# Performance work log

Measured on AMD Instinct MI355X. Metric: run time of the kernel, lower is better.

## Reference

```python
import jax, jax.numpy as jnp
import numpy as np

B, L, D, R = 8, 2048, 2048, 256
K = R if R % 2 == 1 else (R - 1 if R > 1 else 1)  # torch kernel-size rule -> 255


def setup_inputs() -> dict:
    key = jax.random.key(0)
    ks = jax.random.split(key, 6)
    x = jax.random.normal(ks[0], (B, L, D), dtype=jnp.float32)
    ln_gamma = jnp.ones((D,), jnp.float32)
    ln_beta = jnp.zeros((D,), jnp.float32)
    P_shared = jax.random.normal(ks[1], (D, R), jnp.float32) / np.float32(np.sqrt(D))
    dlt_T = jax.random.normal(ks[2], (R, R), jnp.float32) / np.float32(np.sqrt(R))
    phi_w = jax.random.normal(ks[3], (R,), jnp.float32)  # nn.Linear(1, r, bias=False) weight
    phi_bias = jnp.zeros((L, R), jnp.float32)            # created as zeros_like(phi_det)
    toep_params = jnp.ones((K,), jnp.float32) / np.float32(K)
    Wq = jax.random.normal(ks[4], (R, D), jnp.float32) / np.float32(np.sqrt(R))  # delta_Q: r->d
    bq = jnp.zeros((D,), jnp.float32)
    g_logit = jnp.array([-1.0, 0.0], jnp.float32)
    return {"x": x, "ln_gamma": ln_gamma, "ln_beta": ln_beta, "P_shared": P_shared,
            "dlt_T": dlt_T, "phi_w": phi_w, "phi_bias": phi_bias,
            "toep_params": toep_params, "Wq": Wq, "bq": bq, "g_logit": g_logit,
            "step": 5000}


def _layernorm(x, g, b, eps=1e-5):
    m = jnp.mean(x, -1, keepdims=True)
    v = jnp.mean((x - m) ** 2, -1, keepdims=True)
    return (x - m) * jax.lax.rsqrt(v + eps) * g + b


def _phi_det(Ll, Rr, dtype):
    # assumed phi_logic(t, L, r): DCT-II style deterministic phase table, shape (L, r)
    t = jnp.arange(Ll, dtype=dtype)[:, None]
    k = jnp.arange(Rr, dtype=dtype)[None, :]
    return jnp.cos(jnp.pi * (t + 0.5) * k / Ll)


def reference(x, ln_gamma, ln_beta, P_shared, dlt_T, phi_w, phi_bias,
              toep_params, Wq, bq, g_logit, step):
    Bb, Ll, Dd = x.shape
    Rr = P_shared.shape[1]
    x_norm = _layernorm(x, ln_gamma, ln_beta)
    phi_det = _phi_det(Ll, Rr, x.dtype)                      # (L, r)
    feat = jnp.mean(x_norm, -1, keepdims=True)               # (B, L, 1)
    phi_data = jnp.mean(feat * phi_w[None, None, :], axis=0)  # (L, r)
    det_scale = min(step / 2000.0, 1.0)                      # static Python scalar
    phi = det_scale * phi_det + phi_bias + phi_data          # (L, r)
    scale = jnp.sum(phi, axis=1) / jnp.float32(Rr)           # (L,)
    u = jnp.einsum('bld,dr->blr', x_norm, P_shared)          # SharedProj.forward_P
    z = jnp.einsum('blr,sr->bls', u, dlt_T)                  # DLT: fixed spectral transform
    # Toeplitz conv1d across spectral channels, padding 'same' (cross-correlation, as torch)
    zf = z.reshape(Bb * Ll, 1, Rr)
    mixed = jax.lax.conv_general_dilated(zf, toep_params[None, None, :], (1,), 'SAME',
                                         dimension_numbers=('NCH', 'OIH', 'NCH'))
    z_mixed = mixed.reshape(Bb, Ll, Rr)
    y = jnp.einsum('blr,rd->bld', z_mixed, Wq) + bq          # delta_Q
    g = jax.nn.sigmoid(g_logit)
    g = jnp.repeat(g, Dd // g.shape[0])                      # repeat_interleave to d_model
    # scale has L elements, broadcast over the FEATURE dim (L == d_model by construction)
    return g[None, None, :] * y * scale[None, None, :]
```

## Files before the change

### kernel.cpp

```cpp
#include <hip/hip_runtime.h>
#include <cstdint>
#include <math.h>

#define B_ 8
#define L_ 2048
#define D_ 2048
#define R_ 256

typedef __bf16 bf16x8 __attribute__((ext_vector_type(8)));
typedef float f32x4 __attribute__((ext_vector_type(4)));

__device__ __forceinline__ unsigned short f2bf(float f) {
    uint32_t u = __builtin_bit_cast(uint32_t, f);
    u += 0x7FFFu + ((u >> 16) & 1u);
    return (unsigned short)(u >> 16);
}

#define GLDS16(gp, lp)                                                          \
    __builtin_amdgcn_global_load_lds(                                           \
        (const __attribute__((address_space(1))) void*)(gp),                    \
        (__attribute__((address_space(3))) void*)(lp), 16, 0, 0)

__global__ __launch_bounds__(256) void ln_kernel(
    const float* __restrict__ x, const float* __restrict__ gamma,
    const float* __restrict__ beta, unsigned short* __restrict__ xn,
    float* __restrict__ feat)
{
    const int row  = blockIdx.x;
    const int t    = threadIdx.x;
    const int w    = t >> 6, lane = t & 63;
    const float4* x4 = (const float4*)(x + (size_t)row * D_);
    const float4* g4 = (const float4*)gamma;
    const float4* b4 = (const float4*)beta;
    float4 a  = x4[t];
    float4 b  = x4[t + 256];
    float4 g0 = g4[t], g1 = g4[t + 256];
    float4 e0 = b4[t], e1 = b4[t + 256];

    float s   = a.x + a.y + a.z + a.w + b.x + b.y + b.z + b.w;
    float sq  = a.x*a.x + a.y*a.y + a.z*a.z + a.w*a.w
              + b.x*b.x + b.y*b.y + b.z*b.z + b.w*b.w;
    float sxg = a.x*g0.x + a.y*g0.y + a.z*g0.z + a.w*g0.w
              + b.x*g1.x + b.y*g1.y + b.z*g1.z + b.w*g1.w;
    float sg  = g0.x + g0.y + g0.z + g0.w + g1.x + g1.y + g1.z + g1.w;
    float sb  = e0.x + e0.y + e0.z + e0.w + e1.x + e1.y + e1.z + e1.w;

    __shared__ float red[20];
#pragma unroll
    for (int o = 32; o; o >>= 1) {
        s   += __shfl_down(s, o);
        sq  += __shfl_down(sq, o);
        sxg += __shfl_down(sxg, o);
        sg  += __shfl_down(sg, o);
        sb  += __shfl_down(sb, o);
    }
    if (lane == 0) {
        red[w] = s; red[4+w] = sq; red[8+w] = sxg; red[12+w] = sg; red[16+w] = sb;
    }
    __syncthreads();
    float S    = red[0] + red[1] + red[2] + red[3];
    float SQ   = red[4] + red[5] + red[6] + red[7];
    float SXG  = red[8] + red[9] + red[10] + red[11];
    float SG   = red[12] + red[13] + red[14] + red[15];
    float SB   = red[16] + red[17] + red[18] + red[19];
    float mean = S * (1.0f / D_);
    float var  = SQ * (1.0f / D_) - mean * mean;
    float rstd = rsqrtf(var + 1e-5f);
    if (t == 0)
        feat[row] = (rstd * (SXG - mean * SG) + SB) * (1.0f / D_);

    float n[8];
    n[0] = (a.x - mean) * rstd * g0.x + e0.x;
    n[1] = (a.y - mean) * rstd * g0.y + e0.y;
    n[2] = (a.z - mean) * rstd * g0.z + e0.z;
    n[3] = (a.w - mean) * rstd * g0.w + e0.w;
    n[4] = (b.x - mean) * rstd * g1.x + e1.x;
    n[5] = (b.y - mean) * rstd * g1.y + e1.y;
    n[6] = (b.z - mean) * rstd * g1.z + e1.z;
    n[7] = (b.w - mean) * rstd * g1.w + e1.w;

    ushort4 o0, o1;
    o0.x = f2bf(n[0]); o0.y = f2bf(n[1]); o0.z = f2bf(n[2]); o0.w = f2bf(n[3]);
    o1.x = f2bf(n[4]); o1.y = f2bf(n[5]); o1.z = f2bf(n[6]); o1.w = f2bf(n[7]);
    ((ushort4*)(xn + (size_t)row * D_))[t]       = o0;
    ((ushort4*)(xn + (size_t)row * D_))[t + 256] = o1;
}

__global__ __launch_bounds__(256) void pt_kernel(
    const float* __restrict__ P, unsigned short* __restrict__ PT)
{
    __shared__ unsigned short sT[64 * 256];
    const int k0 = blockIdx.x * 64, t = threadIdx.x;
#pragma unroll 8
    for (int j = 0; j < 64; j++)
        sT[j * 256 + t] = f2bf(P[(size_t)(k0 + j) * R_ + t]);
    __syncthreads();
#pragma unroll
    for (int c = 0; c < 16; c++) {
        ushort4 v;
        v.x = sT[(c * 4 + 0) * 256 + t];
        v.y = sT[(c * 4 + 1) * 256 + t];
        v.z = sT[(c * 4 + 2) * 256 + t];
        v.w = sT[(c * 4 + 3) * 256 + t];
        *(ushort4*)(PT + (size_t)t * D_ + k0 + c * 4) = v;
    }
}

__global__ __launch_bounds__(256) void w2_kernel(
    const float* __restrict__ dlt, const float* __restrict__ toep,
    float* __restrict__ W2T)
{
    int s = blockIdx.x, q = threadIdx.x;
    int r0 = s - 127; if (r0 < 0) r0 = 0;
    int r1 = s + 127; if (r1 > 255) r1 = 255;
    float acc = 0.f;
    for (int r = r0; r <= r1; r++)
        acc += dlt[(size_t)r * R_ + q] * toep[r - s + 127];
    W2T[(size_t)s * R_ + q] = acc;
}

__global__ __launch_bounds__(256) void wt_kernel(
    const float* __restrict__ W2T, const float* __restrict__ Wq,
    unsigned short* __restrict__ WT)
{
    const int d0 = blockIdx.x * 4, q = threadIdx.x;
    float a0 = 0.f, a1 = 0.f, a2 = 0.f, a3 = 0.f;
    for (int s = 0; s < R_; s++) {
        float w2 = W2T[(size_t)s * R_ + q];
        const float* wr = Wq + (size_t)s * D_ + d0;
        a0 += w2 * wr[0]; a1 += w2 * wr[1]; a2 += w2 * wr[2]; a3 += w2 * wr[3];
    }
    WT[(size_t)(d0 + 0) * R_ + q] = f2bf(a0);
    WT[(size_t)(d0 + 1) * R_ + q] = f2bf(a1);
    WT[(size_t)(d0 + 2) * R_ + q] = f2bf(a2);
    WT[(size_t)(d0 + 3) * R_ + q] = f2bf(a3);
}

__global__ __launch_bounds__(256) void scale_kernel(
    const float* __restrict__ phi_bias, const float* __restrict__ phi_w,
    const float* __restrict__ feat, const float* __restrict__ bq,
    const float* __restrict__ g_logit, const int* __restrict__ step,
    float* __restrict__ gs, float* __restrict__ bgs)
{
    int l = blockIdx.x, k = threadIdx.x;
    int w = k >> 6, lane = k & 63;
    float arg = 3.14159265358979323846f * ((float)l + 0.5f) * (float)k * (1.0f / L_);
    float cv = cosf(arg);
    float pb = phi_bias[(size_t)l * R_ + k];
    float pw = phi_w[k];
    __shared__ float red[12];
#pragma unroll
    for (int o = 32; o; o >>= 1) {
        cv += __shfl_down(cv, o);
        pb += __shfl_down(pb, o);
        pw += __shfl_down(pw, o);
    }
    if (lane == 0) { red[w] = cv; red[4 + w] = pb; red[8 + w] = pw; }
    __syncthreads();
    if (k == 0) {
        float cs  = red[0] + red[1] + red[2] + red[3];
        float pbs = red[4] + red[5] + red[6] + red[7];
        float pws = red[8] + red[9] + red[10] + red[11];
        float fb = 0.f;
        for (int b = 0; b < B_; b++) fb += feat[(size_t)b * L_ + l];
        fb *= (1.0f / B_);
        float det = fminf((float)step[0] / 2000.0f, 1.0f);
        float sc  = (det * cs + pbs + fb * pws) * (1.0f / R_);
        float gl  = g_logit[l >> 10];
        float gg  = 1.0f / (1.0f + expf(-gl));
        gs[l]  = gg * sc;
        bgs[l] = bq[l] * gg * sc;
    }
}

__global__ __launch_bounds__(256, 2) void gemm1_kernel(
    const unsigned short* __restrict__ A,
    const unsigned short* __restrict__ BT,
    unsigned short* __restrict__ U)
{
    __shared__ __align__(16) unsigned short sA[2][2][128 * 32];
    __shared__ __align__(16) unsigned short sB[2][2][128 * 32];
    const int tid  = threadIdx.x;
    const int n0   = blockIdx.x * 128;
    const int m0   = blockIdx.y * 128;
    const int w    = tid >> 6, lane = tid & 63;
    const int quad = lane >> 4, m16 = lane & 15;
    const int wm   = (w >> 1) * 64, wn = (w & 1) * 64;
    const int ra   = tid >> 2, sa = tid & 3;

    const unsigned short* apb = A  + (size_t)(m0 + ra) * 2048 + sa * 8;
    const unsigned short* bpb = BT + (size_t)(n0 + ra) * 2048 + sa * 8;

    f32x4 acc[4][4] = {};

#define G1_STAGE(buf, kc)                                                       \
    do {                                                                        \
        _Pragma("unroll")                                                       \
        for (int h = 0; h < 2; h++) {                                           \
            GLDS16(apb + (kc) + h * 32,              &sA[buf][h][tid * 8]);     \
            GLDS16(apb + (kc) + h * 32 + 64 * 2048,  &sA[buf][h][2048 + tid * 8]); \
            GLDS16(bpb + (kc) + h * 32,              &sB[buf][h][tid * 8]);     \
            GLDS16(bpb + (kc) + h * 32 + 64 * 2048,  &sB[buf][h][2048 + tid * 8]); \
        }                                                                       \
    } while (0)

    G1_STAGE(0, 0);
    __syncthreads();

    int cur = 0;
    for (int kc = 0; kc < 2048; kc += 64) {
        if (kc + 64 < 2048) G1_STAGE(cur ^ 1, kc + 64);
#pragma unroll
        for (int h = 0; h < 2; h++) {
            bf16x8 af[4], bf[4];
#pragma unroll
            for (int i = 0; i < 4; i++)
                af[i] = *(const bf16x8*)(&sA[cur][h][(wm + i * 16 + m16) * 32 + quad * 8]);
#pragma unroll
            for (int j = 0; j < 4; j++)
                bf[j] = *(const bf16x8*)(&sB[cur][h][(wn + j * 16 + m16) * 32 + quad * 8]);
#pragma unroll
            for (int i = 0; i < 4; i++)
#pragma unroll
                for (int j = 0; j < 4; j++)
                    acc[i][j] = __builtin_amdgcn_mfma_f32_16x16x32_bf16(
                        af[i], bf[j], acc[i][j], 0, 0, 0);
        }
        __syncthreads();
        cur ^= 1;
    }
#undef G1_STAGE

#pragma unroll
    for (int i = 0; i < 4; i++)
#pragma unroll
        for (int j = 0; j < 4; j++) {
            int col = n0 + wn + j * 16 + m16;
#pragma unroll
            for (int r = 0; r < 4; r++) {
                int row = m0 + wm + i * 16 + quad * 4 + r;
                U[(size_t)row * 256 + col] = f2bf(acc[i][j][r]);
            }
        }
}

__global__ __launch_bounds__(256, 3) void gemm2_kernel(
    const unsigned short* __restrict__ A,
    const unsigned short* __restrict__ BT,
    const float* __restrict__ gs, const float* __restrict__ bgs,
    float* __restrict__ out)
{
    __shared__ __align__(16) unsigned short sA[2][128 * 32];
    __shared__ __align__(16) unsigned short sB[2][128 * 32];
    const int tid  = threadIdx.x;
    const int n0   = blockIdx.x * 128;
    const int m0   = blockIdx.y * 128;
    const int w    = tid >> 6, lane = tid & 63;
    const int quad = lane >> 4, m16 = lane & 15;
    const int wm   = (w >> 1) * 64, wn = (w & 1) * 64;
    const int ra   = tid >> 2, sa = tid & 3;

    const unsigned short* apb0 = A  + (size_t)(m0 + ra) * 256 + sa * 8;
    const unsigned short* apb1 = apb0 + (size_t)64 * 256;
    const unsigned short* bpb0 = BT + (size_t)(n0 + ra) * 256 + sa * 8;
    const unsigned short* bpb1 = bpb0 + (size_t)64 * 256;

    float gv[4], bv[4];
#pragma unroll
    for (int j = 0; j < 4; j++) {
        int col = n0 + wn + j * 16 + m16;
        gv[j] = gs[col];
        bv[j] = bgs[col];
    }

    f32x4 acc[4][4] = {};

#define G2_STAGE(buf, kc)                                      \
    do {                                                       \
        GLDS16(apb0 + (kc), &sA[buf][tid * 8]);                \
        GLDS16(apb1 + (kc), &sA[buf][(256 + tid) * 8]);        \
        GLDS16(bpb0 + (kc), &sB[buf][tid * 8]);                \
        GLDS16(bpb1 + (kc), &sB[buf][(256 + tid) * 8]);        \
    } while (0)

    G2_STAGE(0, 0);
    __syncthreads();

    int cur = 0;
    for (int kc = 0; kc < 256; kc += 32) {
        if (kc + 32 < 256) G2_STAGE(cur ^ 1, kc + 32);
        bf16x8 af[4], bf[4];
#pragma unroll
        for (int i = 0; i < 4; i++)
            af[i] = *(const bf16x8*)(&sA[cur][(wm + i * 16 + m16) * 32 + quad * 8]);
#pragma unroll
        for (int j = 0; j < 4; j++)
            bf[j] = *(const bf16x8*)(&sB[cur][(wn + j * 16 + m16) * 32 + quad * 8]);
#pragma unroll
        for (int i = 0; i < 4; i++)
#pragma unroll
            for (int j = 0; j < 4; j++)
                acc[i][j] = __builtin_amdgcn_mfma_f32_16x16x32_bf16(
                    af[i], bf[j], acc[i][j], 0, 0, 0);
        __syncthreads();
        cur ^= 1;
    }
#undef G2_STAGE

#pragma unroll
    for (int i = 0; i < 4; i++)
#pragma unroll
        for (int r = 0; r < 4; r++) {
            int row = m0 + wm + i * 16 + quad * 4 + r;
            float* op = out + (size_t)row * 2048 + n0 + wn;
#pragma unroll
            for (int j = 0; j < 4; j++)
                op[j * 16 + m16] = acc[i][j][r] * gv[j] + bv[j];
        }
}

extern "C" void kernel_launch(void* const* d_in, const int* in_sizes, int n_in,
                              void* d_out, int out_size, void* d_ws, size_t ws_size,
                              hipStream_t stream)
{
    const float* x        = (const float*)d_in[0];
    const float* ln_gamma = (const float*)d_in[1];
    const float* ln_beta  = (const float*)d_in[2];
    const float* P        = (const float*)d_in[3];
    const float* dlt      = (const float*)d_in[4];
    const float* phi_w    = (const float*)d_in[5];
    const float* phi_bias = (const float*)d_in[6];
    const float* toep     = (const float*)d_in[7];
    const float* Wq       = (const float*)d_in[8];
    const float* bq       = (const float*)d_in[9];
    const float* g_logit  = (const float*)d_in[10];
    const int*   step     = (const int*)d_in[11];
    float* out = (float*)d_out;

    char* w = (char*)d_ws;
    unsigned short* xn  = (unsigned short*)(w);
    unsigned short* u   = (unsigned short*)(w + 67108864);
    unsigned short* PT  = (unsigned short*)(w + 75497472);
    unsigned short* WT  = (unsigned short*)(w + 76546048);
    float*          W2T = (float*)(w + 77594624);
    float*          feat= (float*)(w + 77856768);
    float*          gs  = (float*)(w + 77922304);
    float*          bgs = (float*)(w + 77930496);

    ln_kernel<<<dim3(B_ * L_), dim3(256), 0, stream>>>(x, ln_gamma, ln_beta, xn, feat);
    pt_kernel<<<dim3(32), dim3(256), 0, stream>>>(P, PT);
    w2_kernel<<<dim3(R_), dim3(256), 0, stream>>>(dlt, toep, W2T);
    wt_kernel<<<dim3(512), dim3(256), 0, stream>>>(W2T, Wq, WT);
    scale_kernel<<<dim3(L_), dim3(256), 0, stream>>>(phi_bias, phi_w, feat, bq,
                                                     g_logit, step, gs, bgs);
    gemm1_kernel<<<dim3(2, 128), dim3(256), 0, stream>>>(xn, PT, u);
    gemm2_kernel<<<dim3(16, 128), dim3(256), 0, stream>>>(u, WT, gs, bgs, out);
}
```

Baseline: 404.9 us.

## Fuse weight-prep and scale kernels into one launch, reassociate Toeplitz-Wq product

Merges the P transpose, the composed weight computation and the scale computation into a single prep kernel, dispatched by block index. The combined weight is now computed as dlt applied to (Toeplitz times Wq) per 4-column block, which removes the intermediate W2T buffer and its dependent launch. This saves launch overhead and serialization between the small prep kernels. In exchange every block reserves 64KB of shared memory, which can limit how many blocks run at once.

```diff
diff --git a/kernel.cpp b/kernel.cpp
--- a/kernel.cpp
+++ b/kernel.cpp
@@ -86,90 +86,97 @@
     ((ushort4*)(xn + (size_t)row * D_))[t + 256] = o1;
 }
 
-__global__ __launch_bounds__(256) void pt_kernel(
-    const float* __restrict__ P, unsigned short* __restrict__ PT)
-{
-    __shared__ unsigned short sT[64 * 256];
-    const int k0 = blockIdx.x * 64, t = threadIdx.x;
-#pragma unroll 8
-    for (int j = 0; j < 64; j++)
-        sT[j * 256 + t] = f2bf(P[(size_t)(k0 + j) * R_ + t]);
-    __syncthreads();
-#pragma unroll
-    for (int c = 0; c < 16; c++) {
-        ushort4 v;
-        v.x = sT[(c * 4 + 0) * 256 + t];
-        v.y = sT[(c * 4 + 1) * 256 + t];
-        v.z = sT[(c * 4 + 2) * 256 + t];
-        v.w = sT[(c * 4 + 3) * 256 + t];
-        *(ushort4*)(PT + (size_t)t * D_ + k0 + c * 4) = v;
-    }
-}
-
-__global__ __launch_bounds__(256) void w2_kernel(
+__global__ __launch_bounds__(256) void prep_kernel(
+    const float* __restrict__ P, unsigned short* __restrict__ PT,
     const float* __restrict__ dlt, const float* __restrict__ toep,
-    float* __restrict__ W2T)
-{
-    int s = blockIdx.x, q = threadIdx.x;
-    int r0 = s - 127; if (r0 < 0) r0 = 0;
-    int r1 = s + 127; if (r1 > 255) r1 = 255;
-    float acc = 0.f;
-    for (int r = r0; r <= r1; r++)
-        acc += dlt[(size_t)r * R_ + q] * toep[r - s + 127];
-    W2T[(size_t)s * R_ + q] = acc;
-}
-
-__global__ __launch_bounds__(256) void wt_kernel(
-    const float* __restrict__ W2T, const float* __restrict__ Wq,
-    unsigned short* __restrict__ WT)
-{
-    const int d0 = blockIdx.x * 4, q = threadIdx.x;
-    float a0 = 0.f, a1 = 0.f, a2 = 0.f, a3 = 0.f;
-    for (int s = 0; s < R_; s++) {
-        float w2 = W2T[(size_t)s * R_ + q];
-        const float* wr = Wq + (size_t)s * D_ + d0;
-        a0 += w2 * wr[0]; a1 += w2 * wr[1]; a2 += w2 * wr[2]; a3 += w2 * wr[3];
-    }
-    WT[(size_t)(d0 + 0) * R_ + q] = f2bf(a0);
-    WT[(size_t)(d0 + 1) * R_ + q] = f2bf(a1);
-    WT[(size_t)(d0 + 2) * R_ + q] = f2bf(a2);
-    WT[(size_t)(d0 + 3) * R_ + q] = f2bf(a3);
-}
-
-__global__ __launch_bounds__(256) void scale_kernel(
+    const float* __restrict__ Wq, unsigned short* __restrict__ WT,
     const float* __restrict__ phi_bias, const float* __restrict__ phi_w,
     const float* __restrict__ feat, const float* __restrict__ bq,
     const float* __restrict__ g_logit, const int* __restrict__ step,
     float* __restrict__ gs, float* __restrict__ bgs)
 {
-    int l = blockIdx.x, k = threadIdx.x;
-    int w = k >> 6, lane = k & 63;
-    float arg = 3.14159265358979323846f * ((float)l + 0.5f) * (float)k * (1.0f / L_);
-    float cv = cosf(arg);
-    float pb = phi_bias[(size_t)l * R_ + k];
-    float pw = phi_w[k];
-    __shared__ float red[12];
-#pragma unroll
-    for (int o = 32; o; o >>= 1) {
-        cv += __shfl_down(cv, o);
-        pb += __shfl_down(pb, o);
-        pw += __shfl_down(pw, o);
-    }
-    if (lane == 0) { red[w] = cv; red[4 + w] = pb; red[8 + w] = pw; }
-    __syncthreads();
-    if (k == 0) {
-        float cs  = red[0] + red[1] + red[2] + red[3];
-        float pbs = red[4] + red[5] + red[6] + red[7];
-        float pws = red[8] + red[9] + red[10] + red[11];
-        float fb = 0.f;
-        for (int b = 0; b < B_; b++) fb += feat[(size_t)b * L_ + l];
-        fb *= (1.0f / B_);
-        float det = fminf((float)step[0] / 2000.0f, 1.0f);
-        float sc  = (det * cs + pbs + fb * pws) * (1.0f / R_);
-        float gl  = g_logit[l >> 10];
-        float gg  = 1.0f / (1.0f + expf(-gl));
-        gs[l]  = gg * sc;
-        bgs[l] = bq[l] * gg * sc;
+    __shared__ __align__(16) char smem[65536];
+    const int bid = blockIdx.x;
+    const int t   = threadIdx.x;
+
+    if (bid < 32) {
+        unsigned short* sT = (unsigned short*)smem;
+        const int k0 = bid * 64;
+#pragma unroll 8
+        for (int j = 0; j < 64; j++)
+            sT[j * 256 + t] = f2bf(P[(size_t)(k0 + j) * R_ + t]);
+        __syncthreads();
+#pragma unroll
+        for (int c = 0; c < 16; c++) {
+            ushort4 v;
+            v.x = sT[(c * 4 + 0) * 256 + t];
+            v.y = sT[(c * 4 + 1) * 256 + t];
+            v.z = sT[(c * 4 + 2) * 256 + t];
+            v.w = sT[(c * 4 + 3) * 256 + t];
+            *(ushort4*)(PT + (size_t)t * D_ + k0 + c * 4) = v;
+        }
+    } else if (bid < 544) {
+        float* C = (float*)smem;
+        const int d0 = (bid - 32) * 4;
+        {
+            const int r  = t;
+            int s0 = r - 127; if (s0 < 0) s0 = 0;
+            int s1 = r + 127; if (s1 > 255) s1 = 255;
+            float c0 = 0.f, c1 = 0.f, c2 = 0.f, c3 = 0.f;
+            for (int s = s0; s <= s1; s++) {
+                float tv = toep[r - s + 127];
+                const float* wr = Wq + (size_t)s * D_ + d0;
+                c0 += tv * wr[0]; c1 += tv * wr[1];
+                c2 += tv * wr[2]; c3 += tv * wr[3];
+            }
+            C[r * 4 + 0] = c0; C[r * 4 + 1] = c1;
+            C[r * 4 + 2] = c2; C[r * 4 + 3] = c3;
+        }
+        __syncthreads();
+        {
+            const int q = t;
+            float a0 = 0.f, a1 = 0.f, a2 = 0.f, a3 = 0.f;
+            for (int r = 0; r < 256; r++) {
+                float dv = dlt[(size_t)r * R_ + q];
+                a0 += dv * C[r * 4 + 0]; a1 += dv * C[r * 4 + 1];
+                a2 += dv * C[r * 4 + 2]; a3 += dv * C[r * 4 + 3];
+            }
+            WT[(size_t)(d0 + 0) * R_ + q] = f2bf(a0);
+            WT[(size_t)(d0 + 1) * R_ + q] = f2bf(a1);
+            WT[(size_t)(d0 + 2) * R_ + q] = f2bf(a2);
+            WT[(size_t)(d0 + 3) * R_ + q] = f2bf(a3);
+        }
+    } else {
+        float* red = (float*)smem;
+        const int l = bid - 544;
+        const int k = t;
+        const int w = k >> 6, lane = k & 63;
+        float arg = 3.14159265358979323846f * ((float)l + 0.5f) * (float)k * (1.0f / L_);
+        float cv = cosf(arg);
+        float pb = phi_bias[(size_t)l * R_ + k];
+        float pw = phi_w[k];
+#pragma unroll
+        for (int o = 32; o; o >>= 1) {
+            cv += __shfl_down(cv, o);
+            pb += __shfl_down(pb, o);
+            pw += __shfl_down(pw, o);
+        }
+        if (lane == 0) { red[w] = cv; red[4 + w] = pb; red[8 + w] = pw; }
+        __syncthreads();
+        if (k == 0) {
+            float cs  = red[0] + red[1] + red[2] + red[3];
+            float pbs = red[4] + red[5] + red[6] + red[7];
+            float pws = red[8] + red[9] + red[10] + red[11];
+            float fb = 0.f;
+            for (int b = 0; b < B_; b++) fb += feat[(size_t)b * L_ + l];
+            fb *= (1.0f / B_);
+            float det = fminf((float)step[0] / 2000.0f, 1.0f);
+            float sc  = (det * cs + pbs + fb * pws) * (1.0f / R_);
+            float gl  = g_logit[l >> 10];
+            float gg  = 1.0f / (1.0f + expf(-gl));
+            gs[l]  = gg * sc;
+            bgs[l] = bq[l] * gg * sc;
+        }
     }
 }
 
@@ -342,17 +349,14 @@
     unsigned short* u   = (unsigned short*)(w + 67108864);
     unsigned short* PT  = (unsigned short*)(w + 75497472);
     unsigned short* WT  = (unsigned short*)(w + 76546048);
-    float*          W2T = (float*)(w + 77594624);
     float*          feat= (float*)(w + 77856768);
     float*          gs  = (float*)(w + 77922304);
     float*          bgs = (float*)(w + 77930496);
 
     ln_kernel<<<dim3(B_ * L_), dim3(256), 0, stream>>>(x, ln_gamma, ln_beta, xn, feat);
-    pt_kernel<<<dim3(32), dim3(256), 0, stream>>>(P, PT);
-    w2_kernel<<<dim3(R_), dim3(256), 0, stream>>>(dlt, toep, W2T);
-    wt_kernel<<<dim3(512), dim3(256), 0, stream>>>(W2T, Wq, WT);
-    scale_kernel<<<dim3(L_), dim3(256), 0, stream>>>(phi_bias, phi_w, feat, bq,
-                                                     g_logit, step, gs, bgs);
+    prep_kernel<<<dim3(2592), dim3(256), 0, stream>>>(P, PT, dlt, toep, Wq, WT,
+                                                      phi_bias, phi_w, feat, bq,
+                                                      g_logit, step, gs, bgs);
     gemm1_kernel<<<dim3(2, 128), dim3(256), 0, stream>>>(xn, PT, u);
     gemm2_kernel<<<dim3(16, 128), dim3(256), 0, stream>>>(u, WT, gs, bgs, out);
 }
```

After: 406.6 us. About the same (+0.4%).
